# Kernel tuning notes

Measured on AMD Instinct MI355X. Metric: run time of the kernel, lower is better.

## Reference

```python
import jax, jax.numpy as jnp
import numpy as np

EPS = 1e-12  # F.normalize eps

def _layer(x, adj, y, mask, w, b):
    # support = x @ W
    support = x @ w
    a = adj * mask
    # row-wise L1 normalize: a / max(sum|a|, eps)
    norm = jnp.maximum(jnp.sum(jnp.abs(a), axis=1, keepdims=True), EPS)
    a = a / norm
    out = a @ support + b
    y_hat = a @ y
    return out, y_hat

def setup_inputs() -> dict:
    key = jax.random.key(0)
    ks = jax.random.split(key, 9)
    N, F, H, C = 8192, 512, 256, 40
    stdv1 = 1.0 / np.sqrt(H)
    stdv2 = 1.0 / np.sqrt(C)
    return {
        "x": jax.random.normal(ks[0], (N, F), jnp.float32),
        "adj": jax.random.uniform(ks[1], (N, N), jnp.float32),
        "y": jax.random.uniform(ks[2], (N, C), jnp.float32),
        "mask1": jax.random.uniform(ks[3], (N, N), jnp.float32),
        "mask2": jax.random.uniform(ks[4], (N, N), jnp.float32),
        "w1": jax.random.uniform(ks[5], (F, H), jnp.float32, -stdv1, stdv1),
        "b1": jax.random.uniform(ks[6], (H,), jnp.float32, -stdv1, stdv1),
        "w2": jax.random.uniform(ks[7], (H, C), jnp.float32, -stdv2, stdv2),
        "b2": jax.random.uniform(ks[8], (C,), jnp.float32, -stdv2, stdv2),
    }

def reference(x, adj, y, mask1, mask2, w1, b1, w2, b2):
    h, y_hat = _layer(x, adj, y, mask1, w1, b1)
    h = jax.nn.relu(h)  # dropout is identity in eval mode
    h, y_hat = _layer(h, adj, y_hat, mask2, w2, b2)
    return jax.nn.log_softmax(h, axis=1), jax.nn.log_softmax(y_hat, axis=1)
```

## Files before the change

### kernel.cpp

```cpp
#include <hip/hip_runtime.h>
#include <cstdint>
#include <cstddef>

typedef float f32x4 __attribute__((ext_vector_type(4)));
typedef __bf16 bf16x8_t __attribute__((ext_vector_type(8)));
typedef short s16x8_t __attribute__((ext_vector_type(8)));
typedef unsigned short u16x4_t __attribute__((ext_vector_type(4)));

#define NN 8192
#define FD 512
#define HD 256
#define CD 40

static __device__ __forceinline__ unsigned short f2bf(float f) {
    unsigned int u = __builtin_bit_cast(unsigned int, f);
    u += 0x7FFFu + ((u >> 16) & 1u);
    return (unsigned short)(u >> 16);
}
static __device__ __forceinline__ float bf2f(unsigned short s) {
    unsigned int u = ((unsigned int)s) << 16;
    return __builtin_bit_cast(float, u);
}

typedef __attribute__((address_space(3))) unsigned int lds_u32_t;
typedef __attribute__((address_space(1))) const unsigned int gbl_u32_t;
static __device__ __forceinline__ void gload16(const void* g, const void* lds) {
    __builtin_amdgcn_global_load_lds((gbl_u32_t*)g, (lds_u32_t*)lds, 16, 0, 0);
}

__global__ __launch_bounds__(256) void k_prep(const float* __restrict__ adj,
                                              const float* __restrict__ mask1,
                                              const float* __restrict__ mask2,
                                              unsigned short* __restrict__ P1,
                                              unsigned short* __restrict__ P2,
                                              float* __restrict__ sinv1,
                                              float* __restrict__ sinv2) {
    const int row = blockIdx.x;
    const int t = threadIdx.x;
    const f32x4* __restrict__ ar  = (const f32x4*)(adj   + (size_t)row * NN);
    const f32x4* __restrict__ m1r = (const f32x4*)(mask1 + (size_t)row * NN);
    const f32x4* __restrict__ m2r = mask2 ? (const f32x4*)(mask2 + (size_t)row * NN) : nullptr;
    float s1 = 0.f, s2 = 0.f;

    f32x4 a  = __builtin_nontemporal_load(&ar[t]);
    f32x4 m1 = __builtin_nontemporal_load(&m1r[t]);
    f32x4 m2 = {};
    if (m2r) m2 = __builtin_nontemporal_load(&m2r[t]);

    #pragma unroll
    for (int j = 0; j < 8; ++j) {
        const int idx = j * 256 + t;
        f32x4 an = {}, m1n = {}, m2n = {};
        if (j < 7) {
            an  = __builtin_nontemporal_load(&ar[idx + 256]);
            m1n = __builtin_nontemporal_load(&m1r[idx + 256]);
            if (m2r) m2n = __builtin_nontemporal_load(&m2r[idx + 256]);
        }
        {
            const float p0 = a[0] * m1[0], p1 = a[1] * m1[1], p2 = a[2] * m1[2], p3 = a[3] * m1[3];
            s1 += fabsf(p0) + fabsf(p1) + fabsf(p2) + fabsf(p3);
            u16x4_t pk; pk.x = f2bf(p0); pk.y = f2bf(p1); pk.z = f2bf(p2); pk.w = f2bf(p3);
            *(u16x4_t*)&P1[(size_t)row * NN + idx * 4] = pk;
        }
        if (m2r) {
            const float p0 = a[0] * m2[0], p1 = a[1] * m2[1], p2 = a[2] * m2[2], p3 = a[3] * m2[3];
            s2 += fabsf(p0) + fabsf(p1) + fabsf(p2) + fabsf(p3);
            u16x4_t pk; pk.x = f2bf(p0); pk.y = f2bf(p1); pk.z = f2bf(p2); pk.w = f2bf(p3);
            *(u16x4_t*)&P2[(size_t)row * NN + idx * 4] = pk;
        }
        a = an; m1 = m1n; m2 = m2n;
    }
    __shared__ float red1[4], red2[4];
    #pragma unroll
    for (int d = 32; d; d >>= 1) { s1 += __shfl_xor(s1, d, 64); s2 += __shfl_xor(s2, d, 64); }
    if ((t & 63) == 0) { red1[t >> 6] = s1; red2[t >> 6] = s2; }
    __syncthreads();
    if (t == 0) {
        const float a1 = red1[0] + red1[1] + red1[2] + red1[3];
        sinv1[row] = 1.0f / fmaxf(a1, 1e-12f);
        if (sinv2) {
            const float a2 = red2[0] + red2[1] + red2[2] + red2[3];
            sinv2[row] = 1.0f / fmaxf(a2, 1e-12f);
        }
    }
}

__global__ __launch_bounds__(256) void k_xw1(const float* __restrict__ x,
                                             const float* __restrict__ w1,
                                             float* __restrict__ sup1) {
    __shared__ float xs[64][36];
    __shared__ float ws[32][68];
    const int m0 = (blockIdx.x >> 2) * 64;
    const int n0 = (blockIdx.x & 3) * 64;
    const int t = threadIdx.x;
    const int tx = t & 15, ty = t >> 4;
    float acc[4][4] = {};
    for (int k0 = 0; k0 < FD; k0 += 32) {
        for (int i = t; i < 512; i += 256) {
            int r = i >> 3, c = (i & 7) << 2;
            *(float4*)&xs[r][c] = *(const float4*)&x[(size_t)(m0 + r) * FD + k0 + c];
        }
        for (int i = t; i < 512; i += 256) {
            int r = i >> 4, c = (i & 15) << 2;
            *(float4*)&ws[r][c] = *(const float4*)&w1[(size_t)(k0 + r) * HD + n0 + c];
        }
        __syncthreads();
        for (int k = 0; k < 32; ++k) {
            float a_[4], b_[4];
            #pragma unroll
            for (int i = 0; i < 4; ++i) a_[i] = xs[ty * 4 + i][k];
            #pragma unroll
            for (int j = 0; j < 4; ++j) b_[j] = ws[k][tx * 4 + j];
            #pragma unroll
            for (int i = 0; i < 4; ++i)
                #pragma unroll
                for (int j = 0; j < 4; ++j) acc[i][j] += a_[i] * b_[j];
        }
        __syncthreads();
    }
    #pragma unroll
    for (int i = 0; i < 4; ++i)
        #pragma unroll
        for (int j = 0; j < 4; ++j)
            sup1[(size_t)(m0 + ty * 4 + i) * HD + n0 + tx * 4 + j] = acc[i][j];
}

__global__ __launch_bounds__(256) void k_packB1T(const float* __restrict__ sup1,
                                                 const float* __restrict__ y,
                                                 unsigned short* __restrict__ B1T) {
    __shared__ float tl[64][33];
    const int kt = blockIdx.x & 127;
    const int nt = blockIdx.x >> 7;
    const int k0 = kt * 64, n0 = nt * 32;
    const int t = threadIdx.x;
    {
        const int kr = t >> 2, cb = (t & 3) * 8;
        #pragma unroll
        for (int j = 0; j < 8; ++j) {
            const int n = n0 + cb + j;
            float v;
            if (n < 256)      v = sup1[(size_t)(k0 + kr) * HD + n];
            else if (n < 296) v = y[(size_t)(k0 + kr) * CD + (n - 256)];
            else              v = 0.f;
            tl[kr][cb + j] = v;
        }
    }
    __syncthreads();
    {
        const int nr = t >> 3, part = t & 7;
        unsigned short tmp[8];
        #pragma unroll
        for (int j = 0; j < 8; ++j) tmp[j] = f2bf(tl[part * 8 + j][nr]);
        *(s16x8_t*)&B1T[(size_t)(n0 + nr) * NN + k0 + part * 8] = *(s16x8_t*)tmp;
    }
}

template<int BN, int WM, int WN, int SPLIT, int NTILES>
__global__ __launch_bounds__(256) void k_gemm(const unsigned short* __restrict__ A,
                                              const unsigned short* __restrict__ Bt,
                                              float* __restrict__ Cp) {
    constexpr int BM = 128, BK = 64;
    constexpr int MF = BM / (WM * 16);
    constexpr int NF = BN / (WN * 16);
    constexpr int NBI = BN / 32;
    constexpr int NSTR = NTILES * BN;
    constexpr int MT = NN / BM;
    __shared__ unsigned short As[BM * BK];
    __shared__ unsigned short Bs[BN * BK];
    int mt, ks, nt;
    if constexpr (NTILES > 1) {
        constexpr int NXCD = 8;
        constexpr int PAIRS = MT * SPLIT;
        static_assert(PAIRS % NXCD == 0, "pair count must split across XCDs");
        constexpr int PPX = PAIRS / NXCD;
        const int L = blockIdx.x;
        const int x = L % NXCD, q = L / NXCD;
        const int pr = x * PPX + q / NTILES;
        nt = q % NTILES;
        mt = pr / SPLIT;
        ks = pr % SPLIT;
    } else {
        int b = blockIdx.x;
        nt = 0;
        ks = b % SPLIT;  b /= SPLIT;
        mt = b;
    }
    const int m0 = mt * BM, n0 = nt * BN;
    const int t = threadIdx.x, w = t >> 6, ln = t & 63;
    const int wn = w % WN, wm = w / WN;
    const int lrow = ln & 15, lkq = ln >> 4;
    const int kbeg = ks * (NN / SPLIT), kend = kbeg + (NN / SPLIT);

    f32x4 acc[MF][NF] = {};
    for (int kb = kbeg; kb < kend; kb += BK) {
        #pragma unroll
        for (int i = 0; i < 4; ++i) {
            const int off = (w * 4 + i) * 1024 + ln * 16;
            const int r = off >> 7, ch = (off >> 4) & 7;
            gload16(A + (size_t)(m0 + r) * NN + kb + ((ch ^ (r & 7)) << 3),
                    &As[(w * 4 + i) * 512]);
        }
        #pragma unroll
        for (int i = 0; i < NBI; ++i) {
            const int off = (w * NBI + i) * 1024 + ln * 16;
            const int r = off >> 7, ch = (off >> 4) & 7;
            gload16(Bt + (size_t)(n0 + r) * NN + kb + ((ch ^ (r & 7)) << 3),
                    &Bs[(w * NBI + i) * 512]);
        }
        __syncthreads();

        bf16x8_t af[MF][2];
        #pragma unroll
        for (int mf = 0; mf < MF; ++mf)
            #pragma unroll
            for (int kh = 0; kh < 2; ++kh) {
                const int r = wm * (MF * 16) + mf * 16 + lrow;
                const int ch = (kh * 4 + lkq) ^ (r & 7);
                af[mf][kh] = __builtin_bit_cast(bf16x8_t, *(const s16x8_t*)&As[r * 64 + ch * 8]);
            }
        bf16x8_t bfr[NF][2];
        #pragma unroll
        for (int nf = 0; nf < NF; ++nf)
            #pragma unroll
            for (int kh = 0; kh < 2; ++kh) {
                const int r = wn * (NF * 16) + nf * 16 + lrow;
                const int ch = (kh * 4 + lkq) ^ (r & 7);
                bfr[nf][kh] = __builtin_bit_cast(bf16x8_t, *(const s16x8_t*)&Bs[r * 64 + ch * 8]);
            }
        #pragma unroll
        for (int kh = 0; kh < 2; ++kh)
            #pragma unroll
            for (int mf = 0; mf < MF; ++mf)
                #pragma unroll
                for (int nf = 0; nf < NF; ++nf)
                    acc[mf][nf] = __builtin_amdgcn_mfma_f32_16x16x32_bf16(
                        af[mf][kh], bfr[nf][kh], acc[mf][nf], 0, 0, 0);
        __syncthreads();
    }
    #pragma unroll
    for (int mf = 0; mf < MF; ++mf)
        #pragma unroll
        for (int nf = 0; nf < NF; ++nf)
            #pragma unroll
            for (int e = 0; e < 4; ++e) {
                const int m = m0 + wm * (MF * 16) + mf * 16 + lkq * 4 + e;
                const int n = n0 + wn * (NF * 16) + nf * 16 + lrow;
                Cp[((size_t)ks * NN + m) * NSTR + n] = acc[mf][nf][e];
            }
}

__global__ __launch_bounds__(256) void k_finC(const float* __restrict__ U,
                                              const float* __restrict__ sinv1,
                                              const float* __restrict__ b1,
                                              unsigned short* __restrict__ h1,
                                              unsigned short* __restrict__ B2T) {
    const int t = threadIdx.x;
    const int r = t >> 3, l8 = t & 7;
    const int m = blockIdx.x * 32 + r;
    const float si = sinv1[m];
    const float* __restrict__ u0 = U + (size_t)m * 320;
    const float* __restrict__ u1 = U + (size_t)(NN + m) * 320;
    #pragma unroll
    for (int i = 0; i < 10; ++i) {
        const int c = (l8 + i * 8) * 4;
        f32x4 a = *(const f32x4*)&u0[c];
        f32x4 b = *(const f32x4*)&u1[c];
        f32x4 v;
        #pragma unroll
        for (int e = 0; e < 4; ++e) v[e] = (a[e] + b[e]) * si;
        if (i < 8) {
            u16x4_t pk;
            #pragma unroll
            for (int e = 0; e < 4; ++e) {
                const float hv = fmaxf(v[e] + b1[c + e], 0.f);
                ((unsigned short*)&pk)[e] = f2bf(hv);
            }
            *(u16x4_t*)&h1[(size_t)m * HD + c] = pk;
        } else {
            #pragma unroll
            for (int e = 0; e < 4; ++e) {
                const int cc = c + e;
                if (cc < 296) B2T[(size_t)(40 + cc - 256) * NN + m] = f2bf(v[e]);
            }
        }
    }
}

__global__ __launch_bounds__(256) void k_hw2(const unsigned short* __restrict__ h1,
                                             const float* __restrict__ w2,
                                             unsigned short* __restrict__ B2T) {
    __shared__ float w2s[HD * CD];
    __shared__ unsigned short h1s[32][264];
    __shared__ float ot[CD][33];
    const int t = threadIdx.x;
    const int mb = blockIdx.x * 32;
    for (int i = t; i < HD * CD; i += 256) w2s[i] = w2[i];
    for (int i = t; i < 1024; i += 256) {
        const int r = i >> 5, c = (i & 31) * 8;
        *(s16x8_t*)&h1s[r][c] = *(const s16x8_t*)&h1[(size_t)(mb + r) * HD + c];
    }
    __syncthreads();
    const int m = t >> 3, n0 = t & 7;
    float a5[5] = {};
    for (int k = 0; k < HD; ++k) {
        const float hv = bf2f(h1s[m][k]);
        #pragma unroll
        for (int j = 0; j < 5; ++j) a5[j] += hv * w2s[k * CD + n0 + 8 * j];
    }
    #pragma unroll
    for (int j = 0; j < 5; ++j) ot[n0 + 8 * j][m] = a5[j];
    __syncthreads();
    for (int i = t; i < CD * 32; i += 256) {
        const int n = i >> 5, mm = i & 31;
        B2T[(size_t)n * NN + mb + mm] = f2bf(ot[n][mm]);
    }
    for (int i = t; i < 16 * 32; i += 256)
        B2T[(size_t)(80 + (i >> 5)) * NN + mb + (i & 31)] = 0;
}

__global__ __launch_bounds__(256) void k_finD(const float* __restrict__ U,
                                              const float* __restrict__ sinv2,
                                              const float* __restrict__ b2,
                                              float* __restrict__ out) {
    __shared__ float vt[32][100];
    const int t = threadIdx.x;
    const int mb = blockIdx.x * 32;
    for (int i = t; i < 32 * 24; i += 256) {
        const int r = i / 24, f4 = i % 24;
        const int m = mb + r;
        f32x4 s = {};
        #pragma unroll
        for (int p = 0; p < 8; ++p) {
            f32x4 v = *(const f32x4*)&U[((size_t)p * NN + m) * 96 + f4 * 4];
            #pragma unroll
            for (int e = 0; e < 4; ++e) s[e] += v[e];
        }
        const float si = sinv2[m];
        #pragma unroll
        for (int e = 0; e < 4; ++e) {
            const int c = f4 * 4 + e;
            float v = s[e] * si;
            if (c < CD) v += b2[c];
            vt[r][c] = v;
        }
    }
    __syncthreads();
    const int l8 = t & 7;
    #pragma unroll
    for (int pass = 0; pass < 2; ++pass) {
        const int task = pass * 32 + (t >> 3);
        const int row = task & 31, mat = task >> 5;
        float vals[5];
        float mx = -3.0e38f;
        #pragma unroll
        for (int j = 0; j < 5; ++j) { vals[j] = vt[row][mat * CD + l8 + 8 * j]; mx = fmaxf(mx, vals[j]); }
        mx = fmaxf(mx, __shfl_xor(mx, 4, 8));
        mx = fmaxf(mx, __shfl_xor(mx, 2, 8));
        mx = fmaxf(mx, __shfl_xor(mx, 1, 8));
        float se = 0.f;
        #pragma unroll
        for (int j = 0; j < 5; ++j) se += expf(vals[j] - mx);
        se += __shfl_xor(se, 4, 8);
        se += __shfl_xor(se, 2, 8);
        se += __shfl_xor(se, 1, 8);
        const float ls = logf(se);
        float* op = out + (size_t)mat * (NN * CD) + (size_t)(mb + row) * CD;
        #pragma unroll
        for (int j = 0; j < 5; ++j) op[l8 + 8 * j] = vals[j] - mx - ls;
    }
}

extern "C" void kernel_launch(void* const* d_in, const int* in_sizes, int n_in,
                              void* d_out, int out_size, void* d_ws, size_t ws_size,
                              hipStream_t stream) {
    (void)in_sizes; (void)n_in; (void)out_size;
    const float* x     = (const float*)d_in[0];
    const float* adj   = (const float*)d_in[1];
    const float* y     = (const float*)d_in[2];
    const float* mask1 = (const float*)d_in[3];
    const float* mask2 = (const float*)d_in[4];
    const float* w1    = (const float*)d_in[5];
    const float* b1    = (const float*)d_in[6];
    const float* w2    = (const float*)d_in[7];
    const float* b2    = (const float*)d_in[8];
    float* out = (float*)d_out;

    const bool both = ws_size >= 313065472ULL;
    char* p = (char*)d_ws;
    unsigned short* P1 = (unsigned short*)p; p += 134217728;
    unsigned short* P2 = P1;
    if (both) { P2 = (unsigned short*)p; p += 134217728; }
    float*          sup1 = (float*)p;          p += 8388608;
    unsigned short* B1T  = (unsigned short*)p; p += 5242880;
    unsigned short* h1   = (unsigned short*)p; p += 4194304;
    unsigned short* B2T  = (unsigned short*)p; p += 1572864;
    float*          U    = (float*)p;          p += 25165824;
    float*          sinv1 = (float*)p;         p += 32768;
    float*          sinv2 = (float*)p;         p += 32768;

    if (both) {
        hipLaunchKernelGGL(k_prep, dim3(8192), dim3(256), 0, stream,
                           adj, mask1, mask2, P1, P2, sinv1, sinv2);
    } else {
        hipLaunchKernelGGL(k_prep, dim3(8192), dim3(256), 0, stream,
                           adj, mask1, (const float*)nullptr, P1, (unsigned short*)nullptr,
                           sinv1, (float*)nullptr);
    }
    hipLaunchKernelGGL(k_xw1,     dim3(512),  dim3(256), 0, stream, x, w1, sup1);
    hipLaunchKernelGGL(k_packB1T, dim3(1280), dim3(256), 0, stream, sup1, y, B1T);
    hipLaunchKernelGGL(HIP_KERNEL_NAME(k_gemm<64, 2, 2, 2, 5>), dim3(640), dim3(256), 0, stream,
                       P1, B1T, U);
    hipLaunchKernelGGL(k_finC,    dim3(256),  dim3(256), 0, stream, U, sinv1, b1, h1, B2T);
    hipLaunchKernelGGL(k_hw2,     dim3(256),  dim3(256), 0, stream, h1, w2, B2T);
    if (!both) {
        hipLaunchKernelGGL(k_prep, dim3(8192), dim3(256), 0, stream,
                           adj, mask2, (const float*)nullptr, P1, (unsigned short*)nullptr,
                           sinv2, (float*)nullptr);
    }
    hipLaunchKernelGGL(HIP_KERNEL_NAME(k_gemm<96, 4, 1, 8, 1>), dim3(512), dim3(256), 0, stream,
                       P2, B2T, U);
    hipLaunchKernelGGL(k_finD,    dim3(256),  dim3(256), 0, stream, U, sinv2, b2, out);
}
```

Before: 394.9 us.

## Fuse adjacency masking, bf16 conversion and row sums into GEMM loads

Drops the separate prep kernel that wrote masked bf16 copies of adj*mask to workspace. Each GEMM now loads fp32 adj and mask tiles directly, multiplies them, converts to bf16 into swizzled LDS, and builds L1 row sums that are combined with atomics into a zeroed buffer. This removes the large bf16 intermediate writes and re-reads. In exchange, twice as many fp32 bytes are read per tile, the first GEMM re-reads them for each of its five N-tiles, and the register-staged loads are not pipelined.

```diff
diff --git a/kernel.cpp b/kernel.cpp
--- a/kernel.cpp
+++ b/kernel.cpp
@@ -28,61 +28,11 @@
     __builtin_amdgcn_global_load_lds((gbl_u32_t*)g, (lds_u32_t*)lds, 16, 0, 0);
 }
 
-__global__ __launch_bounds__(256) void k_prep(const float* __restrict__ adj,
-                                              const float* __restrict__ mask1,
-                                              const float* __restrict__ mask2,
-                                              unsigned short* __restrict__ P1,
-                                              unsigned short* __restrict__ P2,
-                                              float* __restrict__ sinv1,
-                                              float* __restrict__ sinv2) {
-    const int row = blockIdx.x;
-    const int t = threadIdx.x;
-    const f32x4* __restrict__ ar  = (const f32x4*)(adj   + (size_t)row * NN);
-    const f32x4* __restrict__ m1r = (const f32x4*)(mask1 + (size_t)row * NN);
-    const f32x4* __restrict__ m2r = mask2 ? (const f32x4*)(mask2 + (size_t)row * NN) : nullptr;
-    float s1 = 0.f, s2 = 0.f;
-
-    f32x4 a  = __builtin_nontemporal_load(&ar[t]);
-    f32x4 m1 = __builtin_nontemporal_load(&m1r[t]);
-    f32x4 m2 = {};
-    if (m2r) m2 = __builtin_nontemporal_load(&m2r[t]);
-
-    #pragma unroll
-    for (int j = 0; j < 8; ++j) {
-        const int idx = j * 256 + t;
-        f32x4 an = {}, m1n = {}, m2n = {};
-        if (j < 7) {
-            an  = __builtin_nontemporal_load(&ar[idx + 256]);
-            m1n = __builtin_nontemporal_load(&m1r[idx + 256]);
-            if (m2r) m2n = __builtin_nontemporal_load(&m2r[idx + 256]);
-        }
-        {
-            const float p0 = a[0] * m1[0], p1 = a[1] * m1[1], p2 = a[2] * m1[2], p3 = a[3] * m1[3];
-            s1 += fabsf(p0) + fabsf(p1) + fabsf(p2) + fabsf(p3);
-            u16x4_t pk; pk.x = f2bf(p0); pk.y = f2bf(p1); pk.z = f2bf(p2); pk.w = f2bf(p3);
-            *(u16x4_t*)&P1[(size_t)row * NN + idx * 4] = pk;
-        }
-        if (m2r) {
-            const float p0 = a[0] * m2[0], p1 = a[1] * m2[1], p2 = a[2] * m2[2], p3 = a[3] * m2[3];
-            s2 += fabsf(p0) + fabsf(p1) + fabsf(p2) + fabsf(p3);
-            u16x4_t pk; pk.x = f2bf(p0); pk.y = f2bf(p1); pk.z = f2bf(p2); pk.w = f2bf(p3);
-            *(u16x4_t*)&P2[(size_t)row * NN + idx * 4] = pk;
-        }
-        a = an; m1 = m1n; m2 = m2n;
-    }
-    __shared__ float red1[4], red2[4];
-    #pragma unroll
-    for (int d = 32; d; d >>= 1) { s1 += __shfl_xor(s1, d, 64); s2 += __shfl_xor(s2, d, 64); }
-    if ((t & 63) == 0) { red1[t >> 6] = s1; red2[t >> 6] = s2; }
-    __syncthreads();
-    if (t == 0) {
-        const float a1 = red1[0] + red1[1] + red1[2] + red1[3];
-        sinv1[row] = 1.0f / fmaxf(a1, 1e-12f);
-        if (sinv2) {
-            const float a2 = red2[0] + red2[1] + red2[2] + red2[3];
-            sinv2[row] = 1.0f / fmaxf(a2, 1e-12f);
-        }
-    }
+__global__ __launch_bounds__(256) void k_zero(float* __restrict__ S1,
+                                              float* __restrict__ S2) {
+    const int i = blockIdx.x * 256 + threadIdx.x;
+    S1[i] = 0.f;
+    S2[i] = 0.f;
 }
 
 __global__ __launch_bounds__(256) void k_xw1(const float* __restrict__ x,
@@ -156,9 +106,11 @@
 }
 
 template<int BN, int WM, int WN, int SPLIT, int NTILES>
-__global__ __launch_bounds__(256) void k_gemm(const unsigned short* __restrict__ A,
-                                              const unsigned short* __restrict__ Bt,
-                                              float* __restrict__ Cp) {
+__global__ __launch_bounds__(256) void k_gemmF(const float* __restrict__ adj,
+                                               const float* __restrict__ mask,
+                                               const unsigned short* __restrict__ Bt,
+                                               float* __restrict__ Cp,
+                                               float* __restrict__ S) {
     constexpr int BM = 128, BK = 64;
     constexpr int MF = BM / (WM * 16);
     constexpr int NF = BN / (WN * 16);
@@ -190,15 +142,19 @@
     const int wn = w % WN, wm = w / WN;
     const int lrow = ln & 15, lkq = ln >> 4;
     const int kbeg = ks * (NN / SPLIT), kend = kbeg + (NN / SPLIT);
-
+    const bool dosum = (NTILES == 1) || (nt == 0);
+
+    float rsum[8] = {};
     f32x4 acc[MF][NF] = {};
     for (int kb = kbeg; kb < kend; kb += BK) {
-        #pragma unroll
-        for (int i = 0; i < 4; ++i) {
-            const int off = (w * 4 + i) * 1024 + ln * 16;
-            const int r = off >> 7, ch = (off >> 4) & 7;
-            gload16(A + (size_t)(m0 + r) * NN + kb + ((ch ^ (r & 7)) << 3),
-                    &As[(w * 4 + i) * 512]);
+        f32x4 av[8], mv[8];
+        #pragma unroll
+        for (int i = 0; i < 8; ++i) {
+            const int g = t + i * 256;
+            const int r = g >> 4, q16 = g & 15;
+            const size_t goff = (size_t)(m0 + r) * NN + kb + q16 * 4;
+            av[i] = *(const f32x4*)&adj[goff];
+            mv[i] = *(const f32x4*)&mask[goff];
         }
         #pragma unroll
         for (int i = 0; i < NBI; ++i) {
@@ -206,6 +162,26 @@
             const int r = off >> 7, ch = (off >> 4) & 7;
             gload16(Bt + (size_t)(n0 + r) * NN + kb + ((ch ^ (r & 7)) << 3),
                     &Bs[(w * NBI + i) * 512]);
+        }
+        f32x4 pr8[8];
+        #pragma unroll
+        for (int i = 0; i < 8; ++i) {
+            #pragma unroll
+            for (int e = 0; e < 4; ++e) pr8[i][e] = av[i][e] * mv[i][e];
+        }
+        if (dosum) {
+            #pragma unroll
+            for (int i = 0; i < 8; ++i)
+                rsum[i] += fabsf(pr8[i][0]) + fabsf(pr8[i][1]) + fabsf(pr8[i][2]) + fabsf(pr8[i][3]);
+        }
+        #pragma unroll
+        for (int i = 0; i < 8; ++i) {
+            const int g = t + i * 256;
+            const int r = g >> 4, q16 = g & 15;
+            u16x4_t pk;
+            pk.x = f2bf(pr8[i][0]); pk.y = f2bf(pr8[i][1]);
+            pk.z = f2bf(pr8[i][2]); pk.w = f2bf(pr8[i][3]);
+            *(u16x4_t*)&As[r * 64 + (((q16 >> 1) ^ (r & 7)) << 3) + ((q16 & 1) << 2)] = pk;
         }
         __syncthreads();
 
@@ -247,17 +223,29 @@
                 const int n = n0 + wn * (NF * 16) + nf * 16 + lrow;
                 Cp[((size_t)ks * NN + m) * NSTR + n] = acc[mf][nf][e];
             }
+    if (dosum) {
+        #pragma unroll
+        for (int i = 0; i < 8; ++i) {
+            float v = rsum[i];
+            v += __shfl_xor(v, 1, 64);
+            v += __shfl_xor(v, 2, 64);
+            v += __shfl_xor(v, 4, 64);
+            v += __shfl_xor(v, 8, 64);
+            if ((ln & 15) == 0)
+                atomicAdd(&S[m0 + w * 4 + (ln >> 4) + i * 16], v);
+        }
+    }
 }
 
 __global__ __launch_bounds__(256) void k_finC(const float* __restrict__ U,
-                                              const float* __restrict__ sinv1,
+                                              const float* __restrict__ S1,
                                               const float* __restrict__ b1,
                                               unsigned short* __restrict__ h1,
                                               unsigned short* __restrict__ B2T) {
     const int t = threadIdx.x;
     const int r = t >> 3, l8 = t & 7;
     const int m = blockIdx.x * 32 + r;
-    const float si = sinv1[m];
+    const float si = 1.0f / fmaxf(S1[m], 1e-12f);
     const float* __restrict__ u0 = U + (size_t)m * 320;
     const float* __restrict__ u1 = U + (size_t)(NN + m) * 320;
     #pragma unroll
@@ -319,7 +307,7 @@
 }
 
 __global__ __launch_bounds__(256) void k_finD(const float* __restrict__ U,
-                                              const float* __restrict__ sinv2,
+                                              const float* __restrict__ S2,
                                               const float* __restrict__ b2,
                                               float* __restrict__ out) {
     __shared__ float vt[32][100];
@@ -335,7 +323,7 @@
             #pragma unroll
             for (int e = 0; e < 4; ++e) s[e] += v[e];
         }
-        const float si = sinv2[m];
+        const float si = 1.0f / fmaxf(S2[m], 1e-12f);
         #pragma unroll
         for (int e = 0; e < 4; ++e) {
             const int c = f4 * 4 + e;
@@ -373,7 +361,7 @@
 extern "C" void kernel_launch(void* const* d_in, const int* in_sizes, int n_in,
                               void* d_out, int out_size, void* d_ws, size_t ws_size,
                               hipStream_t stream) {
-    (void)in_sizes; (void)n_in; (void)out_size;
+    (void)in_sizes; (void)n_in; (void)out_size; (void)ws_size;
     const float* x     = (const float*)d_in[0];
     const float* adj   = (const float*)d_in[1];
     const float* y     = (const float*)d_in[2];
@@ -385,39 +373,23 @@
     const float* b2    = (const float*)d_in[8];
     float* out = (float*)d_out;
 
-    const bool both = ws_size >= 313065472ULL;
     char* p = (char*)d_ws;
-    unsigned short* P1 = (unsigned short*)p; p += 134217728;
-    unsigned short* P2 = P1;
-    if (both) { P2 = (unsigned short*)p; p += 134217728; }
     float*          sup1 = (float*)p;          p += 8388608;
     unsigned short* B1T  = (unsigned short*)p; p += 5242880;
     unsigned short* h1   = (unsigned short*)p; p += 4194304;
     unsigned short* B2T  = (unsigned short*)p; p += 1572864;
     float*          U    = (float*)p;          p += 25165824;
-    float*          sinv1 = (float*)p;         p += 32768;
-    float*          sinv2 = (float*)p;         p += 32768;
-
-    if (both) {
-        hipLaunchKernelGGL(k_prep, dim3(8192), dim3(256), 0, stream,
-                           adj, mask1, mask2, P1, P2, sinv1, sinv2);
-    } else {
-        hipLaunchKernelGGL(k_prep, dim3(8192), dim3(256), 0, stream,
-                           adj, mask1, (const float*)nullptr, P1, (unsigned short*)nullptr,
-                           sinv1, (float*)nullptr);
-    }
+    float*          S1   = (float*)p;          p += 32768;
+    float*          S2   = (float*)p;          p += 32768;
+
+    hipLaunchKernelGGL(k_zero,    dim3(32),   dim3(256), 0, stream, S1, S2);
     hipLaunchKernelGGL(k_xw1,     dim3(512),  dim3(256), 0, stream, x, w1, sup1);
     hipLaunchKernelGGL(k_packB1T, dim3(1280), dim3(256), 0, stream, sup1, y, B1T);
-    hipLaunchKernelGGL(HIP_KERNEL_NAME(k_gemm<64, 2, 2, 2, 5>), dim3(640), dim3(256), 0, stream,
-                       P1, B1T, U);
-    hipLaunchKernelGGL(k_finC,    dim3(256),  dim3(256), 0, stream, U, sinv1, b1, h1, B2T);
+    hipLaunchKernelGGL(HIP_KERNEL_NAME(k_gemmF<64, 2, 2, 2, 5>), dim3(640), dim3(256), 0, stream,
+                       adj, mask1, B1T, U, S1);
+    hipLaunchKernelGGL(k_finC,    dim3(256),  dim3(256), 0, stream, U, S1, b1, h1, B2T);
     hipLaunchKernelGGL(k_hw2,     dim3(256),  dim3(256), 0, stream, h1, w2, B2T);
-    if (!both) {
-        hipLaunchKernelGGL(k_prep, dim3(8192), dim3(256), 0, stream,
-                           adj, mask2, (const float*)nullptr, P1, (unsigned short*)nullptr,
-                           sinv2, (float*)nullptr);
-    }
-    hipLaunchKernelGGL(HIP_KERNEL_NAME(k_gemm<96, 4, 1, 8, 1>), dim3(512), dim3(256), 0, stream,
-                       P2, B2T, U);
-    hipLaunchKernelGGL(k_finD,    dim3(256),  dim3(256), 0, stream, U, sinv2, b2, out);
-}
+    hipLaunchKernelGGL(HIP_KERNEL_NAME(k_gemmF<96, 4, 1, 8, 1>), dim3(512), dim3(256), 0, stream,
+                       adj, mask2, B2T, U, S2);
+    hipLaunchKernelGGL(k_finD,    dim3(256),  dim3(256), 0, stream, U, S2, b2, out);
+}
```

After: 493.3 us. 24.9% more time.
